# Kernel tuning notes

Hardware: AMD Instinct MI355X
Metric: run time of the kernel (lower is better)

The kernel has to match this reference:

```python
import jax, jax.numpy as jnp
import numpy as np

EMBED = 1024
HEADS = 16
HEAD_DIM = EMBED // HEADS
N, S = 2, 2048


def setup_inputs() -> dict:
    key = jax.random.key(0)
    ks = jax.random.split(key, 8)
    scale_p = 1.0 / np.sqrt(HEAD_DIM)
    return {
        "queries": jax.random.normal(ks[0], (N, S, EMBED), jnp.float32),
        "keys": jax.random.normal(ks[1], (N, S, EMBED), jnp.float32),
        "values": jax.random.normal(ks[2], (N, S, EMBED), jnp.float32),
        # per-head projection weights, torch Linear convention: y = x @ W.T
        "Wq": jax.random.normal(ks[3], (HEAD_DIM, HEAD_DIM), jnp.float32) * scale_p,
        "Wk": jax.random.normal(ks[4], (HEAD_DIM, HEAD_DIM), jnp.float32) * scale_p,
        "Wv": jax.random.normal(ks[5], (HEAD_DIM, HEAD_DIM), jnp.float32) * scale_p,
        "Wo": jax.random.normal(ks[6], (EMBED, EMBED), jnp.float32) * (1.0 / np.sqrt(EMBED)),
        "bo": jax.random.normal(ks[7], (EMBED,), jnp.float32) * 0.01,
    }


def reference(queries, keys, values, Wq, Wk, Wv, Wo, bo):
    n, sq, e = queries.shape
    sk = keys.shape[1]
    # split heads: (N, S, H, D)
    q = queries.reshape(n, sq, HEADS, HEAD_DIM)
    k = keys.reshape(n, sk, HEADS, HEAD_DIM)
    v = values.reshape(n, sk, HEADS, HEAD_DIM)
    # per-head linear projections (weights shared across heads), torch Linear: x @ W.T
    q = jnp.einsum('nshd,ed->nshe', q, Wq)
    k = jnp.einsum('nshd,ed->nshe', k, Wk)
    v = jnp.einsum('nshd,ed->nshe', v, Wv)
    # attention scores (N, H, Q, K); NOTE: scaled by sqrt(embed_size), as in source
    energy = jnp.einsum('nqhd,nkhd->nhqk', q, k)
    attention = jax.nn.softmax(energy / jnp.sqrt(jnp.float32(EMBED)), axis=3)
    out = jnp.einsum('nhql,nlhd->nqhd', attention, v).reshape(n, sq, EMBED)
    return out @ Wo.T + bo
```

## Files before the change

kernel.cpp:

```cpp
#include <hip/hip_runtime.h>
#include <hip/hip_bf16.h>

#define NB 2
#define SS 2048
#define EE 1024
#define HH 16
#define DD 64
#define NHD (NB*HH)
#define KT 64

#define QSCALE 0.04508422002777998f

typedef _Float16 half8 __attribute__((ext_vector_type(8)));
typedef _Float16 half4 __attribute__((ext_vector_type(4)));
typedef float floatx4 __attribute__((ext_vector_type(4)));

__device__ __forceinline__ half8 cvt8(const float* p) {
    float4 x = *(const float4*)p;
    float4 y = *(const float4*)(p + 4);
    half8 h = { (_Float16)x.x, (_Float16)x.y, (_Float16)x.z, (_Float16)x.w,
                (_Float16)y.x, (_Float16)y.y, (_Float16)y.z, (_Float16)y.w };
    return h;
}

__device__ __forceinline__ int swz64(int row, int colh) {
    return (row << 6) + ((((colh >> 3) ^ (row & 7)) << 3) | (colh & 7));
}

__global__ __launch_bounds__(256) void proj_kernel(
    const float* __restrict__ Q, const float* __restrict__ K, const float* __restrict__ V,
    const float* __restrict__ Wq, const float* __restrict__ Wk, const float* __restrict__ Wv,
    _Float16* __restrict__ Qp, _Float16* __restrict__ Kp, _Float16* __restrict__ Vt)
{
    int t = threadIdx.x, lane = t & 63, wid = t >> 6;
    int lr = lane & 15, lg = lane >> 4;
    int b = blockIdx.x;
    int nh = b >> 5, st = b & 31;
    int n = nh >> 4, h = nh & 15;

    __shared__ __align__(16) _Float16 vt[DD][72];

    const size_t xoff = ((size_t)n * SS + st * 64 + wid * 16 + lr) * EE
                        + (size_t)h * DD + lg * 8;
    const size_t qob = ((size_t)nh * SS + st * 64 + wid * 16 + lg * 4) * DD;

    const float* tens[3] = {Q, K, V};
    const float* wts[3]  = {Wq, Wk, Wv};

    #pragma unroll
    for (int x = 0; x < 3; ++x) {
        const float* Xr = tens[x] + xoff;
        half8 a0 = cvt8(Xr);
        half8 a1 = cvt8(Xr + 32);
        floatx4 acc[4];
        #pragma unroll
        for (int ns = 0; ns < 4; ++ns) {
            const float* Wr = wts[x] + (size_t)(ns * 16 + lr) * DD + lg * 8;
            half8 b0 = cvt8(Wr);
            half8 b1 = cvt8(Wr + 32);
            floatx4 c = (floatx4){0.f, 0.f, 0.f, 0.f};
            c = __builtin_amdgcn_mfma_f32_16x16x32_f16(a0, b0, c, 0, 0, 0);
            c = __builtin_amdgcn_mfma_f32_16x16x32_f16(a1, b1, c, 0, 0, 0);
            acc[ns] = c;
        }
        if (x == 0) {
            #pragma unroll
            for (int ns = 0; ns < 4; ++ns)
                #pragma unroll
                for (int r = 0; r < 4; ++r)
                    Qp[qob + (size_t)r * DD + ns * 16 + lr] = (_Float16)(acc[ns][r] * QSCALE);
        } else if (x == 1) {
            #pragma unroll
            for (int ns = 0; ns < 4; ++ns)
                #pragma unroll
                for (int r = 0; r < 4; ++r)
                    Kp[qob + (size_t)r * DD + ns * 16 + lr] = (_Float16)acc[ns][r];
        } else {
            #pragma unroll
            for (int ns = 0; ns < 4; ++ns)
                #pragma unroll
                for (int r = 0; r < 4; ++r)
                    vt[ns * 16 + lr][wid * 16 + lg * 4 + r] = (_Float16)acc[ns][r];
        }
    }
    __syncthreads();
    {
        int d = t >> 2, q4 = (t & 3) * 16;
        _Float16* dst = Vt + ((size_t)nh * DD + d) * SS + st * 64 + q4;
        *(half8*)dst       = *(const half8*)(&vt[d][q4]);
        *(half8*)(dst + 8) = *(const half8*)(&vt[d][q4 + 8]);
    }
}

__global__ __launch_bounds__(256, 4) void attn_kernel(
    const _Float16* __restrict__ Qp, const _Float16* __restrict__ Kp,
    const _Float16* __restrict__ Vt, _Float16* __restrict__ Of)
{
    int b = blockIdx.x;
    int slot = b >> 3;
    int nh = (b & 7) * 4 + (slot & 3);
    int qt = slot >> 2;
    int n = nh >> 4, h = nh & 15;
    int t = threadIdx.x;
    int lane = t & 63, wid = t >> 6;
    int lr = lane & 15;
    int lg = lane >> 4;

    __shared__ __align__(16) _Float16 kbuf[2][KT * DD];
    __shared__ __align__(16) _Float16 vbuf[2][DD * KT];
    __shared__ __align__(16) _Float16 plds[4][16 * 64];

    const _Float16* Qb = Qp + ((size_t)nh * SS + qt * 64 + wid * 16) * DD;
    const _Float16* Kb = Kp + (size_t)nh * SS * DD;
    const _Float16* Vb = Vt + (size_t)nh * DD * SS;

    half8 qf0 = *(const half8*)(Qb + (size_t)lr * DD + lg * 8);
    half8 qf1 = *(const half8*)(Qb + (size_t)lr * DD + 32 + lg * 8);

    int sr = t >> 3, sc = (t & 7) * 8;

    {
        half8 k0 = *(const half8*)(Kb + (size_t)sr * DD + sc);
        half8 k1 = *(const half8*)(Kb + (size_t)(sr + 32) * DD + sc);
        half8 v0 = *(const half8*)(Vb + (size_t)sr * SS + sc);
        half8 v1 = *(const half8*)(Vb + (size_t)(sr + 32) * SS + sc);
        *(half8*)(&kbuf[0][swz64(sr, sc)]) = k0;
        *(half8*)(&kbuf[0][swz64(sr + 32, sc)]) = k1;
        *(half8*)(&vbuf[0][swz64(sr, sc)]) = v0;
        *(half8*)(&vbuf[0][swz64(sr + 32, sc)]) = v1;
    }
    __syncthreads();

    floatx4 oacc[4];
    #pragma unroll
    for (int ns = 0; ns < 4; ++ns) oacc[ns] = (floatx4){0.f, 0.f, 0.f, 0.f};
    float lsumF = 0.f;

    int p = 0;
    for (int kb = 0; kb < SS; kb += KT, p ^= 1) {
        int kn = (kb + KT) & (SS - 1);
        half8 sk0 = *(const half8*)(Kb + (size_t)(kn + sr) * DD + sc);
        half8 sk1 = *(const half8*)(Kb + (size_t)(kn + sr + 32) * DD + sc);
        half8 sv0 = *(const half8*)(Vb + (size_t)sr * SS + kn + sc);
        half8 sv1 = *(const half8*)(Vb + (size_t)(sr + 32) * SS + kn + sc);

        half8 kf[4][2];
        #pragma unroll
        for (int ns = 0; ns < 4; ++ns) {
            kf[ns][0] = *(const half8*)(&kbuf[p][swz64(ns * 16 + lr, lg * 8)]);
            kf[ns][1] = *(const half8*)(&kbuf[p][swz64(ns * 16 + lr, 32 + lg * 8)]);
        }
        floatx4 sc_[4];
        #pragma unroll
        for (int ns = 0; ns < 4; ++ns) {
            floatx4 c = (floatx4){0.f, 0.f, 0.f, 0.f};
            c = __builtin_amdgcn_mfma_f32_16x16x32_f16(kf[ns][0], qf0, c, 0, 0, 0);
            c = __builtin_amdgcn_mfma_f32_16x16x32_f16(kf[ns][1], qf1, c, 0, 0, 0);
            sc_[ns] = c;
        }
        half8 vf[4][2];
        #pragma unroll
        for (int ns = 0; ns < 4; ++ns) {
            vf[ns][0] = *(const half8*)(&vbuf[p][swz64(ns * 16 + lr, lg * 8)]);
            vf[ns][1] = *(const half8*)(&vbuf[p][swz64(ns * 16 + lr, 32 + lg * 8)]);
        }
        #pragma unroll
        for (int ns = 0; ns < 4; ++ns) {
            float p0 = exp2f(fminf(sc_[ns][0], 50.f));
            float p1 = exp2f(fminf(sc_[ns][1], 50.f));
            float p2 = exp2f(fminf(sc_[ns][2], 50.f));
            float p3 = exp2f(fminf(sc_[ns][3], 50.f));
            lsumF += (p0 + p1) + (p2 + p3);
            half4 v = { (_Float16)p0, (_Float16)p1, (_Float16)p2, (_Float16)p3 };
            *(half4*)(&plds[wid][swz64(lr, ns * 16 + lg * 4)]) = v;
        }
        asm volatile("s_waitcnt lgkmcnt(0)" ::: "memory");
        half8 pf0 = *(const half8*)(&plds[wid][swz64(lr, lg * 8)]);
        half8 pf1 = *(const half8*)(&plds[wid][swz64(lr, 32 + lg * 8)]);
        #pragma unroll
        for (int ns = 0; ns < 4; ++ns) {
            oacc[ns] = __builtin_amdgcn_mfma_f32_16x16x32_f16(pf0, vf[ns][0], oacc[ns], 0, 0, 0);
            oacc[ns] = __builtin_amdgcn_mfma_f32_16x16x32_f16(pf1, vf[ns][1], oacc[ns], 0, 0, 0);
        }
        *(half8*)(&kbuf[p ^ 1][swz64(sr, sc)]) = sk0;
        *(half8*)(&kbuf[p ^ 1][swz64(sr + 32, sc)]) = sk1;
        *(half8*)(&vbuf[p ^ 1][swz64(sr, sc)]) = sv0;
        *(half8*)(&vbuf[p ^ 1][swz64(sr + 32, sc)]) = sv1;
        __syncthreads();
    }

    float s = lsumF;
    s += __shfl_xor(s, 16, 64);
    s += __shfl_xor(s, 32, 64);
    float linv[4];
    #pragma unroll
    for (int r = 0; r < 4; ++r)
        linv[r] = 1.f / __shfl(s, lg * 4 + r, 64);

    _Float16* Ob = Of + ((size_t)n * SS + qt * 64 + wid * 16) * EE + h * DD;
    #pragma unroll
    for (int ns = 0; ns < 4; ++ns)
        #pragma unroll
        for (int r = 0; r < 4; ++r)
            Ob[(size_t)(lg * 4 + r) * EE + ns * 16 + lr] = (_Float16)(oacc[ns][r] * linv[r]);
}

__global__ __launch_bounds__(256) void wconv_kernel(
    const float* __restrict__ W, _Float16* __restrict__ Wf)
{
    int i = (blockIdx.x * 256 + threadIdx.x) * 8;
    *(half8*)(Wf + i) = cvt8(W + i);
}

__global__ __launch_bounds__(256, 1) void oproj_kernel(
    const _Float16* __restrict__ Of, const _Float16* __restrict__ Wf,
    const float* __restrict__ bo, float* __restrict__ out)
{
    int b = blockIdx.x;
    int nb = b & 7, mb = b >> 3;
    int t = threadIdx.x, lane = t & 63, wid = t >> 6;
    int wm = wid >> 1, wn = wid & 1;
    int lr = lane & 15, lg = lane >> 4;
    int m0 = mb * 128, n0 = nb * 128;

    __shared__ __align__(16) _Float16 As[2][128][72];
    __shared__ __align__(16) _Float16 Bs[2][128][72];

    int srow = t >> 1, scol = (t & 1) * 32;
    const _Float16* Ag = Of + (size_t)(m0 + srow) * EE + scol;
    const _Float16* Bg = Wf + (size_t)(n0 + srow) * EE + scol;

    floatx4 acc[4][4];
    #pragma unroll
    for (int sm = 0; sm < 4; ++sm)
        #pragma unroll
        for (int sn = 0; sn < 4; ++sn) acc[sm][sn] = (floatx4){0.f, 0.f, 0.f, 0.f};

    #pragma unroll
    for (int j = 0; j < 4; ++j) {
        *(half8*)(&As[0][srow][scol + j * 8]) = *(const half8*)(Ag + j * 8);
        *(half8*)(&Bs[0][srow][scol + j * 8]) = *(const half8*)(Bg + j * 8);
    }
    __syncthreads();

    int p = 0;
    for (int kb = 0; kb < EE; kb += 64, p ^= 1) {
        int kn = kb + 64;
        half8 sa[4], sb[4];
        if (kn < EE) {
            #pragma unroll
            for (int j = 0; j < 4; ++j) {
                sa[j] = *(const half8*)(Ag + kn + j * 8);
                sb[j] = *(const half8*)(Bg + kn + j * 8);
            }
        }
        #pragma unroll
        for (int kk = 0; kk < 2; ++kk) {
            half8 af[4], bf[4];
            #pragma unroll
            for (int s = 0; s < 4; ++s) {
                af[s] = *(const half8*)(&As[p][wm * 64 + s * 16 + lr][kk * 32 + lg * 8]);
                bf[s] = *(const half8*)(&Bs[p][wn * 64 + s * 16 + lr][kk * 32 + lg * 8]);
            }
            #pragma unroll
            for (int sm = 0; sm < 4; ++sm)
                #pragma unroll
                for (int sn = 0; sn < 4; ++sn)
                    acc[sm][sn] = __builtin_amdgcn_mfma_f32_16x16x32_f16(
                        af[sm], bf[sn], acc[sm][sn], 0, 0, 0);
        }
        if (kn < EE) {
            #pragma unroll
            for (int j = 0; j < 4; ++j) {
                *(half8*)(&As[p ^ 1][srow][scol + j * 8]) = sa[j];
                *(half8*)(&Bs[p ^ 1][srow][scol + j * 8]) = sb[j];
            }
        }
        __syncthreads();
    }

    #pragma unroll
    for (int sn = 0; sn < 4; ++sn) {
        int nn = n0 + wn * 64 + sn * 16 + lr;
        float bn = bo[nn];
        #pragma unroll
        for (int sm = 0; sm < 4; ++sm) {
            #pragma unroll
            for (int r = 0; r < 4; ++r)
                out[(size_t)(m0 + wm * 64 + sm * 16 + lg * 4 + r) * EE + nn]
                    = acc[sm][sn][r] + bn;
        }
    }
}

extern "C" void kernel_launch(void* const* d_in, const int* in_sizes, int n_in,
                              void* d_out, int out_size, void* d_ws, size_t ws_size,
                              hipStream_t stream)
{
    const float* Q  = (const float*)d_in[0];
    const float* K  = (const float*)d_in[1];
    const float* V  = (const float*)d_in[2];
    const float* Wq = (const float*)d_in[3];
    const float* Wk = (const float*)d_in[4];
    const float* Wv = (const float*)d_in[5];
    const float* Wo = (const float*)d_in[6];
    const float* bo = (const float*)d_in[7];
    float* out = (float*)d_out;

    const size_t NSE = (size_t)NB * SS * EE;
    _Float16* Qp = (_Float16*)d_ws;
    _Float16* Kp = Qp + NSE;
    _Float16* Vt = Kp + NSE;
    _Float16* Of = Vt + NSE;
    _Float16* Wf = Of + NSE;

    proj_kernel<<<1024, 256, 0, stream>>>(Q, K, V, Wq, Wk, Wv, Qp, Kp, Vt);
    wconv_kernel<<<(EE * EE) / (256 * 8), 256, 0, stream>>>(Wo, Wf);
    attn_kernel<<<NHD * (SS / 64), 256, 0, stream>>>(Qp, Kp, Vt, Of);
    oproj_kernel<<<256, 256, 0, stream>>>(Of, Wf, bo, out);
}
```

Measured before the change: 211.8 us.

## Compute softmax row sums via MFMA, pack fp16 with cvt_pkrtz, retile output projection

In the attention kernel, the per-thread scalar sum of exponentials and the final cross-lane shuffles are replaced by an MFMA of the probability fragments against a ones vector. That row sum then lands in the same accumulator layout as the output. Probabilities are packed to fp16 with the packed round-toward-zero convert, which differs slightly in rounding. The output projection GEMM moves from 128x128 to 64x128 tiles with 512 blocks and launch bounds allowing 2 blocks per CU, to improve occupancy and CU coverage on the 256-CU device.

```diff
diff --git a/kernel.cpp b/kernel.cpp
--- a/kernel.cpp
+++ b/kernel.cpp
@@ -21,6 +21,10 @@
     half8 h = { (_Float16)x.x, (_Float16)x.y, (_Float16)x.z, (_Float16)x.w,
                 (_Float16)y.x, (_Float16)y.y, (_Float16)y.z, (_Float16)y.w };
     return h;
+}
+
+__device__ __forceinline__ unsigned int pkrtz_u32(float a, float b) {
+    return __builtin_bit_cast(unsigned int, __builtin_amdgcn_cvt_pkrtz(a, b));
 }
 
 __device__ __forceinline__ int swz64(int row, int colh) {
@@ -117,6 +121,9 @@
     half8 qf0 = *(const half8*)(Qb + (size_t)lr * DD + lg * 8);
     half8 qf1 = *(const half8*)(Qb + (size_t)lr * DD + 32 + lg * 8);
 
+    half8 ones = { (_Float16)1.f, (_Float16)1.f, (_Float16)1.f, (_Float16)1.f,
+                   (_Float16)1.f, (_Float16)1.f, (_Float16)1.f, (_Float16)1.f };
+
     int sr = t >> 3, sc = (t & 7) * 8;
 
     {
@@ -134,7 +141,7 @@
     floatx4 oacc[4];
     #pragma unroll
     for (int ns = 0; ns < 4; ++ns) oacc[ns] = (floatx4){0.f, 0.f, 0.f, 0.f};
-    float lsumF = 0.f;
+    floatx4 sacc = (floatx4){0.f, 0.f, 0.f, 0.f};
 
     int p = 0;
     for (int kb = 0; kb < SS; kb += KT, p ^= 1) {
@@ -170,9 +177,10 @@
             float p1 = exp2f(fminf(sc_[ns][1], 50.f));
             float p2 = exp2f(fminf(sc_[ns][2], 50.f));
             float p3 = exp2f(fminf(sc_[ns][3], 50.f));
-            lsumF += (p0 + p1) + (p2 + p3);
-            half4 v = { (_Float16)p0, (_Float16)p1, (_Float16)p2, (_Float16)p3 };
-            *(half4*)(&plds[wid][swz64(lr, ns * 16 + lg * 4)]) = v;
+            uint2 pr;
+            pr.x = pkrtz_u32(p0, p1);
+            pr.y = pkrtz_u32(p2, p3);
+            *(uint2*)(&plds[wid][swz64(lr, ns * 16 + lg * 4)]) = pr;
         }
         asm volatile("s_waitcnt lgkmcnt(0)" ::: "memory");
         half8 pf0 = *(const half8*)(&plds[wid][swz64(lr, lg * 8)]);
@@ -182,6 +190,8 @@
             oacc[ns] = __builtin_amdgcn_mfma_f32_16x16x32_f16(pf0, vf[ns][0], oacc[ns], 0, 0, 0);
             oacc[ns] = __builtin_amdgcn_mfma_f32_16x16x32_f16(pf1, vf[ns][1], oacc[ns], 0, 0, 0);
         }
+        sacc = __builtin_amdgcn_mfma_f32_16x16x32_f16(pf0, ones, sacc, 0, 0, 0);
+        sacc = __builtin_amdgcn_mfma_f32_16x16x32_f16(pf1, ones, sacc, 0, 0, 0);
         *(half8*)(&kbuf[p ^ 1][swz64(sr, sc)]) = sk0;
         *(half8*)(&kbuf[p ^ 1][swz64(sr + 32, sc)]) = sk1;
         *(half8*)(&vbuf[p ^ 1][swz64(sr, sc)]) = sv0;
@@ -189,13 +199,10 @@
         __syncthreads();
     }
 
-    float s = lsumF;
-    s += __shfl_xor(s, 16, 64);
-    s += __shfl_xor(s, 32, 64);
     float linv[4];
     #pragma unroll
     for (int r = 0; r < 4; ++r)
-        linv[r] = 1.f / __shfl(s, lg * 4 + r, 64);
+        linv[r] = 1.f / sacc[r];
 
     _Float16* Ob = Of + ((size_t)n * SS + qt * 64 + wid * 16) * EE + h * DD;
     #pragma unroll
@@ -212,58 +219,60 @@
     *(half8*)(Wf + i) = cvt8(W + i);
 }
 
-__global__ __launch_bounds__(256, 1) void oproj_kernel(
+__global__ __launch_bounds__(256, 2) void oproj_kernel(
     const _Float16* __restrict__ Of, const _Float16* __restrict__ Wf,
     const float* __restrict__ bo, float* __restrict__ out)
 {
     int b = blockIdx.x;
-    int nb = b & 7, mb = b >> 3;
+    int mb = b & 63, nb = b >> 6;
     int t = threadIdx.x, lane = t & 63, wid = t >> 6;
     int wm = wid >> 1, wn = wid & 1;
     int lr = lane & 15, lg = lane >> 4;
-    int m0 = mb * 128, n0 = nb * 128;
-
-    __shared__ __align__(16) _Float16 As[2][128][72];
+    int m0 = mb * 64, n0 = nb * 128;
+
+    __shared__ __align__(16) _Float16 As[2][64][72];
     __shared__ __align__(16) _Float16 Bs[2][128][72];
 
-    int srow = t >> 1, scol = (t & 1) * 32;
-    const _Float16* Ag = Of + (size_t)(m0 + srow) * EE + scol;
-    const _Float16* Bg = Wf + (size_t)(n0 + srow) * EE + scol;
-
-    floatx4 acc[4][4];
-    #pragma unroll
-    for (int sm = 0; sm < 4; ++sm)
+    int arow = t >> 2, acol = (t & 3) * 16;
+    int brow = t >> 1, bcol = (t & 1) * 32;
+    const _Float16* Ag = Of + (size_t)(m0 + arow) * EE + acol;
+    const _Float16* Bg = Wf + (size_t)(n0 + brow) * EE + bcol;
+
+    floatx4 acc[2][4];
+    #pragma unroll
+    for (int sm = 0; sm < 2; ++sm)
         #pragma unroll
         for (int sn = 0; sn < 4; ++sn) acc[sm][sn] = (floatx4){0.f, 0.f, 0.f, 0.f};
 
     #pragma unroll
-    for (int j = 0; j < 4; ++j) {
-        *(half8*)(&As[0][srow][scol + j * 8]) = *(const half8*)(Ag + j * 8);
-        *(half8*)(&Bs[0][srow][scol + j * 8]) = *(const half8*)(Bg + j * 8);
-    }
+    for (int j = 0; j < 2; ++j)
+        *(half8*)(&As[0][arow][acol + j * 8]) = *(const half8*)(Ag + j * 8);
+    #pragma unroll
+    for (int j = 0; j < 4; ++j)
+        *(half8*)(&Bs[0][brow][bcol + j * 8]) = *(const half8*)(Bg + j * 8);
     __syncthreads();
 
     int p = 0;
     for (int kb = 0; kb < EE; kb += 64, p ^= 1) {
         int kn = kb + 64;
-        half8 sa[4], sb[4];
+        half8 sa[2], sb[4];
         if (kn < EE) {
             #pragma unroll
-            for (int j = 0; j < 4; ++j) {
-                sa[j] = *(const half8*)(Ag + kn + j * 8);
-                sb[j] = *(const half8*)(Bg + kn + j * 8);
-            }
+            for (int j = 0; j < 2; ++j) sa[j] = *(const half8*)(Ag + kn + j * 8);
+            #pragma unroll
+            for (int j = 0; j < 4; ++j) sb[j] = *(const half8*)(Bg + kn + j * 8);
         }
         #pragma unroll
         for (int kk = 0; kk < 2; ++kk) {
-            half8 af[4], bf[4];
-            #pragma unroll
-            for (int s = 0; s < 4; ++s) {
-                af[s] = *(const half8*)(&As[p][wm * 64 + s * 16 + lr][kk * 32 + lg * 8]);
+            half8 af[2], bf[4];
+            #pragma unroll
+            for (int s = 0; s < 2; ++s)
+                af[s] = *(const half8*)(&As[p][wm * 32 + s * 16 + lr][kk * 32 + lg * 8]);
+            #pragma unroll
+            for (int s = 0; s < 4; ++s)
                 bf[s] = *(const half8*)(&Bs[p][wn * 64 + s * 16 + lr][kk * 32 + lg * 8]);
-            }
-            #pragma unroll
-            for (int sm = 0; sm < 4; ++sm)
+            #pragma unroll
+            for (int sm = 0; sm < 2; ++sm)
                 #pragma unroll
                 for (int sn = 0; sn < 4; ++sn)
                     acc[sm][sn] = __builtin_amdgcn_mfma_f32_16x16x32_f16(
@@ -271,10 +280,11 @@
         }
         if (kn < EE) {
             #pragma unroll
-            for (int j = 0; j < 4; ++j) {
-                *(half8*)(&As[p ^ 1][srow][scol + j * 8]) = sa[j];
-                *(half8*)(&Bs[p ^ 1][srow][scol + j * 8]) = sb[j];
-            }
+            for (int j = 0; j < 2; ++j)
+                *(half8*)(&As[p ^ 1][arow][acol + j * 8]) = sa[j];
+            #pragma unroll
+            for (int j = 0; j < 4; ++j)
+                *(half8*)(&Bs[p ^ 1][brow][bcol + j * 8]) = sb[j];
         }
         __syncthreads();
     }
@@ -284,10 +294,10 @@
         int nn = n0 + wn * 64 + sn * 16 + lr;
         float bn = bo[nn];
         #pragma unroll
-        for (int sm = 0; sm < 4; ++sm) {
+        for (int sm = 0; sm < 2; ++sm) {
             #pragma unroll
             for (int r = 0; r < 4; ++r)
-                out[(size_t)(m0 + wm * 64 + sm * 16 + lg * 4 + r) * EE + nn]
+                out[(size_t)(m0 + wm * 32 + sm * 16 + lg * 4 + r) * EE + nn]
                     = acc[sm][sn][r] + bn;
         }
     }
@@ -317,5 +327,5 @@
     proj_kernel<<<1024, 256, 0, stream>>>(Q, K, V, Wq, Wk, Wv, Qp, Kp, Vt);
     wconv_kernel<<<(EE * EE) / (256 * 8), 256, 0, stream>>>(Wo, Wf);
     attn_kernel<<<NHD * (SS / 64), 256, 0, stream>>>(Qp, Kp, Vt, Of);
-    oproj_kernel<<<256, 256, 0, stream>>>(Of, Wf, bo, out);
-}
+    oproj_kernel<<<512, 256, 0, stream>>>(Of, Wf, bo, out);
+}
```

After: 207.9 us. No clear change (-1.8%).
